# Kernel optimization log

Measured on AMD Instinct MI355X. Metric: run time of the kernel, lower is better.

## Reference

```python
import jax, jax.numpy as jnp
import numpy as np

N_OBJS = 100          # max detections / scatter buffer size
TOP_K = 100           # top_k_n peaks per channel
KP_THRES = 0.3        # score threshold before NMS
NMS_IOU = 0.5
RESIZE_H, RESIZE_W = 1536.0, 1536.0   # resize_shape (== heatmap HxW here)
H, W = 1536, 1536


def _peak_hms(hms):
    # 3x3 stride-1 SAME max pool; keep only local maxima (Base.apply_max_pool)
    hmax = jax.lax.reduce_window(hms, -jnp.inf, jax.lax.max, (1, 3, 3, 1), (1, 1, 1, 1), 'SAME')
    return jnp.where(hms == hmax, hms, 0.0)


def _top_k_loc(hms, k):
    # per-channel top-k peak coordinates -> [b, c, k, 2] (y, x) int32
    b, h, w, c = hms.shape
    flat = jnp.transpose(hms, (0, 3, 1, 2)).reshape(b, c, h * w)
    _, idx = jax.lax.top_k(flat, k)
    return jnp.stack([idx // w, idx % w], axis=-1).astype(jnp.int32)


def _iou_matrix(boxes):
    # boxes [N,4] = (y1,x1,y2,x2)
    y1, x1, y2, x2 = boxes[:, 0], boxes[:, 1], boxes[:, 2], boxes[:, 3]
    area = jnp.maximum(y2 - y1, 0.0) * jnp.maximum(x2 - x1, 0.0)
    iy1 = jnp.maximum(y1[:, None], y1[None, :]); ix1 = jnp.maximum(x1[:, None], x1[None, :])
    iy2 = jnp.minimum(y2[:, None], y2[None, :]); ix2 = jnp.minimum(x2[:, None], x2[None, :])
    inter = jnp.maximum(iy2 - iy1, 0.0) * jnp.maximum(ix2 - ix1, 0.0)
    union = area[:, None] + area[None, :] - inter
    return inter / jnp.maximum(union, 1e-8)


def _nms_single(boxes, scores):
    # greedy single-class NMS, fixed-size (combined_non_max_suppression equivalent,
    # clip_boxes=False, score_threshold=-inf); padded slots are zeros like TF.
    order = jnp.argsort(-scores)
    boxes, scores = boxes[order], scores[order]
    n = boxes.shape[0]
    iou = _iou_matrix(boxes)
    idxs = jnp.arange(n)

    def step(suppressed, inp):
        i, iou_row = inp
        keep_i = ~suppressed[i]
        return suppressed | (keep_i & (iou_row > NMS_IOU) & (idxs > i)), keep_i

    _, keep = jax.lax.scan(step, jnp.zeros(n, bool), (idxs, iou))
    perm = jnp.argsort(jnp.where(keep, 0, 1))  # stable: compact kept to front, score order preserved
    keep_s = keep[perm]
    out_boxes = jnp.where(keep_s[:, None], boxes[perm], 0.0)
    out_scores = jnp.where(keep_s, scores[perm], 0.0)
    return out_boxes, out_scores, jnp.zeros(n, jnp.float32)


def _forward(obj_heat_map, offset_map, size_maps, origin_shapes):
    resize_shape = jnp.array([RESIZE_H, RESIZE_W], jnp.float32)
    ratio = origin_shapes / resize_shape                      # [b,2]
    hms = _peak_hms(obj_heat_map)                             # [b,H,W,2]
    b = hms.shape[0]
    coors = _top_k_loc(hms, TOP_K)                            # [b,2,K,2]
    b_coors, b_lnmks = coors[:, :1], coors[:, 1:]             # obj / nose coords
    bidx = jnp.arange(b)[:, None, None]

    # nose landmark: scores at nose-channel peaks, masked mean of coords (int mean like TF)
    nose_scores = hms[bidx, b_lnmks[..., 0], b_lnmks[..., 1], 1]     # [b,1,K]
    nose_mask = nose_scores > 0.5
    cnt = jnp.maximum(jnp.sum(nose_mask), 1)
    lnmk_mean = jnp.sum(jnp.where(nose_mask[..., None], b_lnmks, 0), axis=(0, 1, 2)) // cnt
    b_lnmks_m = lnmk_mean.reshape(b, 1, 2)                    # requires b == 1 (as in original)
    b_nose_scores = jnp.where(nose_mask, nose_scores, -1.0).reshape(b, -1)

    # boxes from sizes at object peaks
    size_vals = size_maps[bidx, b_coors[..., 0], b_coors[..., 1]]    # [b,1,K,2]
    obj_scores = hms[bidx, b_coors[..., 0], b_coors[..., 1], 0]      # [b,1,K]
    centers = b_coors.astype(jnp.float32)
    tls = jnp.maximum(centers - size_vals / 2.0, 0.0)
    brs = jnp.minimum(centers + size_vals / 2.0, resize_shape - 1.0)
    bboxes = jnp.concatenate([tls, brs], axis=-1) * jnp.tile(ratio, (1, 2))[:, None, None, :]
    bboxes, scores = bboxes[:, 0], obj_scores[:, 0]           # [b,K,4], [b,K]

    # scatter masked candidates into -1-initialized buffer (tensor_scatter_nd_update equivalent)
    mask = scores > KP_THRES
    cand = jnp.where(mask[..., None], jnp.concatenate([bboxes, scores[..., None]], -1), -1.0)
    cand = jnp.pad(cand, ((0, 0), (0, N_OBJS - TOP_K), (0, 0)), constant_values=-1.0)  # [b,N_OBJS,5]

    nb, ns, nc = jax.vmap(_nms_single)(cand[..., :4], cand[..., 4])
    box_results = jnp.where(nb == -1.0, jnp.inf, nb)
    box_results = jnp.where(box_results == 0.0, jnp.inf, box_results)  # (x - 1 == -1)
    b_bboxes = jnp.concatenate([box_results, ns[..., None], nc[..., None]], axis=-1)  # [b,N_OBJS,6]

    # offset vectors at the mean nose landmark (gather 8ch -> [b,n,4,2])
    bidx2 = jnp.arange(b)[:, None]
    off = offset_map[bidx2, b_lnmks_m[..., 0], b_lnmks_m[..., 1]].reshape(b, 1, 4, 2)
    lf = b_lnmks_m.astype(jnp.float32)
    b_ENM = (lf[:, :, None, :] - off) * ratio[:, None, None, :]
    b_lnmks_out = lf * ratio[:, None, :]
    return b_bboxes, b_lnmks_out, b_ENM, b_nose_scores


def setup_inputs() -> dict:
    key = jax.random.key(0)
    k1, k2, k3 = jax.random.split(key, 3)
    obj_heat_map = jax.random.uniform(k1, (1, H, W, 2), jnp.float32)
    offset_map = jax.random.normal(k2, (1, H, W, 8), jnp.float32) * 8.0
    size_maps = jax.random.uniform(k3, (1, H, W, 2), jnp.float32) * 128.0
    origin_shapes = jnp.array([[1080.0, 1920.0]], jnp.float32)
    return {"obj_heat_map": obj_heat_map, "offset_map": offset_map,
            "size_maps": size_maps, "origin_shapes": origin_shapes}


def reference(obj_heat_map, offset_map, size_maps, origin_shapes):
    return _forward(obj_heat_map, offset_map, size_maps, origin_shapes)
```

## Files before the change

kernel.cpp:

```cpp
#include <hip/hip_runtime.h>
#include <cstdint>

#define IW 1536
#define IH 1536
#define TOPK 100
#define CAPP 327680
#define CAPB 128
#define CAPM 32768
#define BF_INF16 0x7F7Fu

typedef unsigned u32; typedef unsigned long long u64; typedef unsigned short u16;

#define OH1   0
#define OCNT  4096
#define OSEL  4100
#define OPK   4104
#define OPV   (OPK + 2*CAPP)
#define OMID  (OPV + CAPP)

__device__ __forceinline__ u32 enc16(u32 b){ b &= 0xFFFFu; return (b & 0x8000u) ? ((~b)&0xFFFFu) : (b|0x8000u); }
__device__ __forceinline__ u32 dec16(u32 e){ return (e & 0x8000u) ? (e^0x8000u) : ((~e)&0xFFFFu); }
__device__ __forceinline__ float up16(u32 b){ return __uint_as_float((b&0xFFFFu)<<16); }
__device__ __forceinline__ u16 f2bf(float f){ u32 u=__float_as_uint(f); return (u16)((u + 0x7FFFu + ((u>>16)&1u))>>16); }

__device__ __forceinline__ void wave_sel2048(const u32* bins, u32 need, int* Dout, u32* Aout){
  int lane = threadIdx.x & 63;
  u32 s = 0;
  #pragma unroll
  for(int k=0;k<32;++k) s += bins[lane*32+k];
  u32 c = s;
  #pragma unroll
  for(int off=1;off<64;off<<=1){
    u32 v = __shfl_down(c, off, 64);
    if(lane + off < 64) c += v;
  }
  u32 cnext = __shfl_down(c, 1, 64); if(lane==63) cnext = 0u;
  u64 m = __ballot(c >= need);
  if(m == 0ull){ if(lane==0){ *Dout = 0; *Aout = 0u; } return; }
  int L = 63 - __builtin_clzll((unsigned long long)m);
  if(lane == L){
    u32 above = cnext; int D = 32*L;
    for(int b=32*L+31; b>=32*L; --b){
      u32 h = bins[b];
      if(above + h >= need){ D = b; break; }
      above += h;
    }
    *Dout = D; *Aout = above;
  }
}

__global__ __launch_bounds__(1024) void scan_kernel(const u32* __restrict__ hm, u32* __restrict__ ws){
  __shared__ u32 lh[4096];
  __shared__ u32 lbuf[2][1600];
  __shared__ u16 vbuf[2][1600];
  __shared__ u32 lcnt[2], lbase[2];
  int tid = threadIdx.x, lane = tid & 63;
  for(int i=tid;i<4096;i+=1024) lh[i]=0u;
  if(tid<2) lcnt[tid]=0u;
  __syncthreads();

  int p = (blockIdx.x*1024 + tid)*4;
  int y = p / IW, x = p - y*IW;
  const u32* R1 = hm + y*IW;
  const u32* R0 = y ? R1 - IW : R1;
  const u32* R2 = (y < IH-1) ? R1 + IW : R1;
  uint4 c0 = *(const uint4*)(R0+x), c1 = *(const uint4*)(R1+x), c2 = *(const uint4*)(R2+x);
  int xl = x ? x-1 : 0, xr = (x+4 < IW) ? x+4 : IW-1;
  u32 a0[6] = {R0[xl], c0.x, c0.y, c0.z, c0.w, R0[xr]};
  u32 a1[6] = {R1[xl], c1.x, c1.y, c1.z, c1.w, R1[xr]};
  u32 a2[6] = {R2[xl], c2.x, c2.y, c2.z, c2.w, R2[xr]};

  #pragma unroll
  for(int j=0;j<4;++j){
    u32 cc = a1[j+1];
    u32 cl = cc & 0xFFFFu, chv = cc >> 16;
    u32 m0=0u, m1=0u;
    #pragma unroll
    for(int d=0;d<3;++d){
      u32 n0=a0[j+d], n2=a2[j+d]; u32 t;
      t=n0&0xFFFFu; m0=t>m0?t:m0;  t=n0>>16; m1=t>m1?t:m1;
      t=n2&0xFFFFu; m0=t>m0?t:m0;  t=n2>>16; m1=t>m1?t:m1;
    }
    { u32 n=a1[j];   u32 t=n&0xFFFFu; m0=t>m0?t:m0; t=n>>16; m1=t>m1?t:m1; }
    { u32 n=a1[j+2]; u32 t=n&0xFFFFu; m0=t>m0?t:m0; t=n>>16; m1=t>m1?t:m1; }
    bool pk0 = (cl >= m0), pk1 = (chv >= m1);
    u32 idx = (u32)(p + j);

    u64 mk0 = __ballot(pk0);
    if(mk0){
      u32 cw = __popcll(mk0), b;
      if(lane==0) b = atomicAdd(&lcnt[0], cw);
      b = __shfl(b, 0);
      if(pk0){
        u32 pos = b + __popcll(mk0 & ((1ull<<lane)-1ull));
        if(pos < 1600){ lbuf[0][pos] = idx; vbuf[0][pos] = (u16)cl; }
      }
    }
    u64 mk1 = __ballot(pk1);
    if(mk1){
      u32 cw = __popcll(mk1), b;
      if(lane==0) b = atomicAdd(&lcnt[1], cw);
      b = __shfl(b, 0);
      if(pk1){
        u32 pos = b + __popcll(mk1 & ((1ull<<lane)-1ull));
        if(pos < 1600){ lbuf[1][pos] = idx; vbuf[1][pos] = (u16)chv; }
      }
    }
    if(pk0) atomicAdd(&lh[enc16(cl)>>5], 1u);
    if(pk1) atomicAdd(&lh[2048 + (enc16(chv)>>5)], 1u);
  }
  __syncthreads();
  if(tid < 2){
    u32 n = lcnt[tid]; if(n > 1600) n = 1600;
    lcnt[tid] = n;
    lbase[tid] = atomicAdd(&ws[OCNT+tid], n);
  }
  __syncthreads();
  u16* pv = (u16*)(ws + OPV);
  for(int ch=0;ch<2;++ch){
    u32 n = lcnt[ch], base = lbase[ch];
    for(u32 i=tid;i<n;i+=1024){
      u32 g = base + i;
      if(g < CAPP){ ws[OPK + ch*CAPP + g] = lbuf[ch][i]; pv[ch*CAPP + g] = vbuf[ch][i]; }
    }
  }
  for(int i=tid;i<4096;i+=1024) if(lh[i]) atomicAdd(&ws[OH1+i], lh[i]);
}

#define GRID2 128
__global__ __launch_bounds__(1024) void mid_kernel(u32* __restrict__ ws){
  __shared__ u32 lhh[4096];
  __shared__ u64 mbuf[2][2048];
  __shared__ u32 mcnt[2], mbase[2];
  __shared__ int Dsh[2]; __shared__ u32 Ash[2];
  int tid = threadIdx.x, lane = tid & 63;
  for(int i=tid;i<4096;i+=1024) lhh[i] = ws[OH1+i];
  if(tid < 2) mcnt[tid] = 0u;
  __syncthreads();
  if(tid < 64)                wave_sel2048(lhh,        (u32)TOPK, &Dsh[0], &Ash[0]);
  else if(tid < 128)          wave_sel2048(lhh + 2048, (u32)TOPK, &Dsh[1], &Ash[1]);
  __syncthreads();
  if(blockIdx.x == 0 && tid < 2){ ws[OSEL+tid] = (u32)Dsh[tid]; ws[OSEL+2+tid] = Ash[tid]; }

  const u16* pv = (const u16*)(ws + OPV);
  for(int ch=0;ch<2;++ch){
    u32 n = ws[OCNT+ch]; if(n > CAPP) n = CAPP;
    int D = Dsh[ch];
    for(u32 base = blockIdx.x*1024; base < n; base += GRID2*1024){
      u32 i = base + tid;
      bool act = (i < n);
      u32 e = 0, idx = 0;
      if(act){ e = enc16(pv[ch*CAPP + i]); idx = ws[OPK + ch*CAPP + i]; }
      bool hit = act && ((int)(e>>5) >= D);
      u64 mk = __ballot(hit);
      if(mk){
        u32 cw = __popcll(mk), b;
        if(lane==0) b = atomicAdd(&mcnt[ch], cw);
        b = __shfl(b, 0);
        if(hit){
          u32 pos = b + __popcll(mk & ((1ull<<lane)-1ull));
          if(pos < 2048) mbuf[ch][pos] = ((u64)e<<32) | (u32)(~idx);
        }
      }
    }
  }
  __syncthreads();
  if(tid < 2){
    u32 c = mcnt[tid]; if(c > 2048) c = 2048;
    mcnt[tid] = c;
    mbase[tid] = atomicAdd(&ws[OCNT+2+tid], c);
  }
  __syncthreads();
  u64* mid = (u64*)(ws + OMID);
  for(int ch=0;ch<2;++ch)
    for(u32 i=tid;i<mcnt[ch];i+=1024){
      u32 g = mbase[ch] + i;
      if(g < CAPM) mid[ch*CAPM + g] = mbuf[ch][i];
    }
}

__global__ __launch_bounds__(1024) void finalize_kernel(
    u32* __restrict__ ws, const u32* __restrict__ szm, const u16* __restrict__ offm,
    const u16* __restrict__ orig, u16* __restrict__ out){
  __shared__ u64 keys[CAPB];
  __shared__ u32 lsdw[16][32];
  __shared__ u32 lsd[32];
  __shared__ u32 h2[2048];
  __shared__ u32 wbits[64];
  __shared__ u32 sel[CAPB];
  __shared__ int Bv, selc, selc2, Lsh;
  __shared__ float oval[TOPK]; __shared__ int oidx[TOPK];
  __shared__ float nval[TOPK]; __shared__ int nidx[TOPK];
  __shared__ float cbox[TOPK][4]; __shared__ float cscore[TOPK]; __shared__ float area[TOPK];
  __shared__ int sup[TOPK]; __shared__ int slotv[TOPK];
  __shared__ u64 nbits[2*TOPK];
  __shared__ u64 suppS[2];
  __shared__ int cS, srS, scS, meanr, meanc;
  int tid = threadIdx.x, lane = tid & 63, wid = tid >> 6;

  if(tid < TOPK){ oval[tid]=0.0f; oidx[tid]=0; nval[tid]=0.0f; nidx[tid]=0; }
  __syncthreads();

  for(int ch=0; ch<2; ++ch){
    int nM = (int)ws[OCNT+2+ch]; if(nM > CAPM) nM = CAPM;
    int D = (int)ws[OSEL+ch];
    u32 above = ws[OSEL+2+ch];
    const u64* mid = ((const u64*)(ws + OMID)) + ch*CAPM;
    float* dval = ch ? nval : oval;
    int*   didx = ch ? nidx : oidx;

    for(int i=tid;i<2048;i+=1024) h2[i]=0u;
    if(tid < 512) ((u32*)lsdw)[tid] = 0u;
    if(tid < 64) wbits[tid]=0u;
    if(tid == 0){ selc = 0; selc2 = 0; Bv = 0; Lsh = 0; }
    __syncthreads();

    for(int i=tid;i<nM;i+=1024){
      u64 k = mid[i]; u32 e = (u32)(k>>32);
      if((int)(e>>5) > D){
        int pos = atomicAdd(&selc, 1); if(pos < CAPB) keys[pos] = k;
      } else {
        atomicAdd(&lsdw[wid][e & 31u], 1u);
      }
    }
    __syncthreads();
    if(tid < 32){
      u32 s = 0;
      #pragma unroll
      for(int w=0;w<16;++w) s += lsdw[w][tid];
      lsd[tid] = s;
    }
    __syncthreads();
    if(tid == 0){
      u32 need2 = (u32)TOPK - above;
      u32 a2 = 0; int L = 0;
      for(int b=31;b>=1;--b){
        u32 h = lsd[b];
        if(a2 + h >= need2){ L = b; break; }
        a2 += h;
      }
      Lsh = L;
    }
    __syncthreads();
    u32 thr = ((u32)D<<5) | (u32)Lsh;
    float tval = up16(dec16(thr));

    for(int i=tid;i<nM;i+=1024){
      u64 k = mid[i]; u32 e = (u32)(k>>32);
      if(e > thr && (e>>5) == (u32)D){
        int pos = atomicAdd(&selc, 1); if(pos < CAPB) keys[pos] = k;
      } else if(e == thr){
        u32 idx = ~(u32)(k & 0xFFFFFFFFu);
        atomicAdd(&h2[idx>>11], 1u);
      }
    }
    __syncthreads();
    int nA = selc; if(nA > CAPB) nA = CAPB; if(nA > TOPK) nA = TOPK;
    if(tid < nA){
      u64 kreg = keys[tid];
      int r = 0;
      for(int j=0;j<nA;++j) r += (keys[j] > kreg);
      if(r < TOPK){
        dval[r] = up16(dec16((u32)(kreg>>32)));
        didx[r] = (int)(~(u32)(kreg & 0xFFFFFFFFu));
      }
    }
    int need = TOPK - nA;

    if(need > 0){
      if(tid < 64){
        int base = tid*32;
        u32 s = 0;
        #pragma unroll
        for(int k2=0;k2<32;++k2) s += h2[base+k2];
        u32 c = s;
        #pragma unroll
        for(int off=1;off<64;off<<=1){
          u32 v = __shfl_up(c, off, 64);
          if(lane >= off) c += v;
        }
        u64 m = __ballot(c >= (u32)need);
        int L = (int)(__ffsll((unsigned long long)m) - 1);
        if(tid == L){
          u32 cum2 = c - s;
          int B = base;
          for(int k2=0;k2<32;++k2){
            u32 hb = h2[base+k2];
            if(cum2 + hb >= (u32)need){ B = base+k2; break; }
            cum2 += hb;
          }
          Bv = B;
        }
      }
      __syncthreads();
      int B = Bv;
      for(int i=tid;i<nM;i+=1024){
        u64 k = mid[i]; u32 e = (u32)(k>>32);
        if(e == thr){
          u32 idx = ~(u32)(k & 0xFFFFFFFFu);
          int b = (int)(idx>>11);
          if(b < B){
            int pos = atomicAdd(&selc2, 1);
            if(pos < CAPB) sel[pos] = idx;
          } else if(b == B){
            atomicOr(&wbits[(idx&2047)>>5], 1u<<(idx&31));
          }
        }
      }
      __syncthreads();
      int sc = selc2; if(sc > CAPB) sc = CAPB;
      if(tid < sc){
        u32 v = sel[tid];
        int r = 0;
        for(int j=0;j<sc;++j) r += (sel[j] < v);
        if(nA + r < TOPK){ dval[nA+r] = tval; didx[nA+r] = (int)v; }
      }
      if(tid == 0){
        int rem = need - sc;
        int pos = nA + sc;
        for(int wi=0; wi<64 && rem>0; ++wi){
          u32 bits = wbits[wi];
          while(bits && rem>0){
            int l = __ffs(bits) - 1;
            bits &= bits - 1;
            if(pos < TOPK){ dval[pos] = tval; didx[pos] = (int)(((u32)Bv<<11) | ((u32)wi<<5) | (u32)l); }
            ++pos; --rem;
          }
        }
      }
    }
    __syncthreads();
  }

  float ry = up16(orig[0]) / 1536.0f;
  float rx = up16(orig[1]) / 1536.0f;

  if(tid == 0){ cS = 0; srS = 0; scS = 0; }
  __syncthreads();
  if(tid < TOPK && nval[tid] > 0.5f){
    atomicAdd(&cS, 1);
    atomicAdd(&srS, nidx[tid] / IW);
    atomicAdd(&scS, nidx[tid] % IW);
  }
  if(tid < TOPK) out[610 + tid] = f2bf(nval[tid] > 0.5f ? nval[tid] : -1.0f);
  __syncthreads();
  if(tid == 0){
    int c = cS < 1 ? 1 : cS;
    meanr = srS / c; meanc = scS / c;
  }

  if(tid < TOPK){
    int idx = oidx[tid];
    int r = idx / IW, c = idx - r*IW;
    float score = oval[tid];
    u32 sz = szm[idx];
    float sy = up16(sz), sx = up16(sz>>16);
    float cy = (float)r, cx = (float)c;
    float tly = fmaxf(cy - sy*0.5f, 0.0f);
    float tlx = fmaxf(cx - sx*0.5f, 0.0f);
    float bry = fminf(cy + sy*0.5f, 1535.0f);
    float brx = fminf(cx + sx*0.5f, 1535.0f);
    bool mk = score > 0.3f;
    float b0 = mk ? tly*ry : -1.0f;
    float b1 = mk ? tlx*rx : -1.0f;
    float b2 = mk ? bry*ry : -1.0f;
    float b3 = mk ? brx*rx : -1.0f;
    cbox[tid][0]=b0; cbox[tid][1]=b1; cbox[tid][2]=b2; cbox[tid][3]=b3;
    cscore[tid] = mk ? score : -1.0f;
    area[tid] = fmaxf(b2-b0,0.0f) * fmaxf(b3-b1,0.0f);
  }
  if(tid < 2*TOPK) nbits[tid] = 0ull;
  __syncthreads();

  for(int t=tid; t<TOPK*TOPK; t+=1024){
    int i = t / TOPK, j = t - i*TOPK;
    if(j > i){
      float iy1 = fmaxf(cbox[i][0], cbox[j][0]);
      float ix1 = fmaxf(cbox[i][1], cbox[j][1]);
      float iy2 = fminf(cbox[i][2], cbox[j][2]);
      float ix2 = fminf(cbox[i][3], cbox[j][3]);
      float inter = fmaxf(iy2-iy1,0.0f) * fmaxf(ix2-ix1,0.0f);
      float uni = (area[i] + area[j]) - inter;
      if(inter / fmaxf(uni, 1e-8f) > 0.5f)
        atomicOr(&nbits[i*2 + (j>>6)], 1ull << (j&63));
    }
  }
  __syncthreads();
  if(tid == 0){
    u64 s0 = 0ull, s1 = 0ull;
    for(int i=0;i<TOPK;++i){
      bool su = (i<64) ? ((s0>>i)&1ull) : ((s1>>(i-64))&1ull);
      if(!su){ s0 |= nbits[i*2]; s1 |= nbits[i*2+1]; }
    }
    suppS[0] = s0; suppS[1] = s1;
  }
  __syncthreads();
  if(tid < TOPK) sup[tid] = (int)((suppS[tid>>6] >> (tid&63)) & 1ull);
  __syncthreads();

  if(tid < TOPK){
    int kbefore = 0, sbefore = 0, ktot = 0;
    for(int j=0;j<TOPK;++j){
      int sj = sup[j];
      ktot += (1 - sj);
      if(j < tid){ kbefore += (1 - sj); sbefore += sj; }
    }
    int slot = sup[tid] ? (ktot + sbefore) : kbefore;
    slotv[slot] = tid;
  }
  __syncthreads();

  if(tid < TOPK){
    int s = slotv[tid];
    bool ks = !sup[s];
    u16 row[6];
    if(ks){
      for(int d=0;d<4;++d){
        float v = cbox[s][d];
        row[d] = (v == -1.0f || v == 0.0f) ? (u16)BF_INF16 : f2bf(v);
      }
      row[4] = f2bf(cscore[s]);
    } else {
      for(int d=0;d<4;++d) row[d] = (u16)BF_INF16;
      row[4] = 0;
    }
    row[5] = 0;
    for(int d=0;d<6;++d) out[tid*6 + d] = row[d];
  }

  if(tid == 0){
    float lfy = (float)meanr, lfx = (float)meanc;
    out[600] = f2bf(lfy * ry);
    out[601] = f2bf(lfx * rx);
    const u16* op = offm + ((size_t)meanr*IW + meanc)*8;
    for(int p=0;p<4;++p){
      out[602 + p*2 + 0] = f2bf((lfy - up16(op[p*2+0])) * ry);
      out[602 + p*2 + 1] = f2bf((lfx - up16(op[p*2+1])) * rx);
    }
  }
}

extern "C" void kernel_launch(void* const* d_in, const int* in_sizes, int n_in,
                              void* d_out, int out_size, void* d_ws, size_t ws_size,
                              hipStream_t stream) {
  const u32* heat = (const u32*)d_in[0];
  const u16* offm = (const u16*)d_in[1];
  const u32* szm  = (const u32*)d_in[2];
  const u16* orig = (const u16*)d_in[3];
  u16* out = (u16*)d_out;
  u32* ws = (u32*)d_ws;

  hipMemsetAsync(ws, 0, 4104*sizeof(u32), stream);
  scan_kernel<<<576, 1024, 0, stream>>>(heat, ws);
  mid_kernel<<<GRID2, 1024, 0, stream>>>(ws);
  finalize_kernel<<<1, 1024, 0, stream>>>(ws, szm, offm, orig, out);
}
```

Before: 200.3 us.

## Split mid candidates into above-digit list and tie list with global low-digit histogram

After: 199.3 us. No clear change (-0.5%).

```diff
diff --git a/kernel.cpp b/kernel.cpp
--- a/kernel.cpp
+++ b/kernel.cpp
@@ -6,17 +6,20 @@
 #define TOPK 100
 #define CAPP 327680
 #define CAPB 128
-#define CAPM 32768
+#define CAPT 8192
 #define BF_INF16 0x7F7Fu
 
 typedef unsigned u32; typedef unsigned long long u64; typedef unsigned short u16;
 
 #define OH1   0
 #define OCNT  4096
-#define OSEL  4100
-#define OPK   4104
+#define OSEL  4102
+#define OLSD  4106
+#define OZEND 4172
+#define OPK   4172
 #define OPV   (OPK + 2*CAPP)
-#define OMID  (OPV + CAPP)
+#define OLB   (OPV + CAPP)
+#define OLT   (OLB + 4*CAPB)
 
 __device__ __forceinline__ u32 enc16(u32 b){ b &= 0xFFFFu; return (b & 0x8000u) ? ((~b)&0xFFFFu) : (b|0x8000u); }
 __device__ __forceinline__ u32 dec16(u32 e){ return (e & 0x8000u) ? (e^0x8000u) : ((~e)&0xFFFFu); }
@@ -130,19 +133,22 @@
 #define GRID2 128
 __global__ __launch_bounds__(1024) void mid_kernel(u32* __restrict__ ws){
   __shared__ u32 lhh[4096];
-  __shared__ u64 mbuf[2][2048];
-  __shared__ u32 mcnt[2], mbase[2];
+  __shared__ u64 tbuf[2][2048];
+  __shared__ u32 tcnt[2], tbase[2];
+  __shared__ u32 lsdl[64];
   __shared__ int Dsh[2]; __shared__ u32 Ash[2];
   int tid = threadIdx.x, lane = tid & 63;
   for(int i=tid;i<4096;i+=1024) lhh[i] = ws[OH1+i];
-  if(tid < 2) mcnt[tid] = 0u;
-  __syncthreads();
-  if(tid < 64)                wave_sel2048(lhh,        (u32)TOPK, &Dsh[0], &Ash[0]);
-  else if(tid < 128)          wave_sel2048(lhh + 2048, (u32)TOPK, &Dsh[1], &Ash[1]);
+  if(tid < 2) tcnt[tid] = 0u;
+  if(tid < 64) lsdl[tid] = 0u;
+  __syncthreads();
+  if(tid < 64)       wave_sel2048(lhh,        (u32)TOPK, &Dsh[0], &Ash[0]);
+  else if(tid < 128) wave_sel2048(lhh + 2048, (u32)TOPK, &Dsh[1], &Ash[1]);
   __syncthreads();
   if(blockIdx.x == 0 && tid < 2){ ws[OSEL+tid] = (u32)Dsh[tid]; ws[OSEL+2+tid] = Ash[tid]; }
 
   const u16* pv = (const u16*)(ws + OPV);
+  u64* listB = (u64*)(ws + OLB);
   for(int ch=0;ch<2;++ch){
     u32 n = ws[OCNT+ch]; if(n > CAPP) n = CAPP;
     int D = Dsh[ch];
@@ -151,40 +157,45 @@
       bool act = (i < n);
       u32 e = 0, idx = 0;
       if(act){ e = enc16(pv[ch*CAPP + i]); idx = ws[OPK + ch*CAPP + i]; }
-      bool hit = act && ((int)(e>>5) >= D);
-      u64 mk = __ballot(hit);
+      if(act && (int)(e>>5) > D){
+        u32 pos = atomicAdd(&ws[OCNT+2+ch], 1u);
+        if(pos < CAPB) listB[ch*CAPB + pos] = ((u64)e<<32) | (u32)(~idx);
+      }
+      bool isT = act && ((int)(e>>5) == D);
+      if(isT) atomicAdd(&lsdl[ch*32 + (e & 31u)], 1u);
+      u64 mk = __ballot(isT);
       if(mk){
         u32 cw = __popcll(mk), b;
-        if(lane==0) b = atomicAdd(&mcnt[ch], cw);
+        if(lane==0) b = atomicAdd(&tcnt[ch], cw);
         b = __shfl(b, 0);
-        if(hit){
+        if(isT){
           u32 pos = b + __popcll(mk & ((1ull<<lane)-1ull));
-          if(pos < 2048) mbuf[ch][pos] = ((u64)e<<32) | (u32)(~idx);
+          if(pos < 2048) tbuf[ch][pos] = ((u64)e<<32) | (u32)(~idx);
         }
       }
     }
   }
   __syncthreads();
   if(tid < 2){
-    u32 c = mcnt[tid]; if(c > 2048) c = 2048;
-    mcnt[tid] = c;
-    mbase[tid] = atomicAdd(&ws[OCNT+2+tid], c);
-  }
-  __syncthreads();
-  u64* mid = (u64*)(ws + OMID);
+    u32 c = tcnt[tid]; if(c > 2048) c = 2048;
+    tcnt[tid] = c;
+    tbase[tid] = atomicAdd(&ws[OCNT+4+tid], c);
+  }
+  __syncthreads();
+  u64* tie = (u64*)(ws + OLT);
   for(int ch=0;ch<2;++ch)
-    for(u32 i=tid;i<mcnt[ch];i+=1024){
-      u32 g = mbase[ch] + i;
-      if(g < CAPM) mid[ch*CAPM + g] = mbuf[ch][i];
-    }
+    for(u32 i=tid;i<tcnt[ch];i+=1024){
+      u32 g = tbase[ch] + i;
+      if(g < CAPT) tie[ch*CAPT + g] = tbuf[ch][i];
+    }
+  if(tid < 64 && lsdl[tid]) atomicAdd(&ws[OLSD + tid], lsdl[tid]);
 }
 
-__global__ __launch_bounds__(1024) void finalize_kernel(
+__global__ __launch_bounds__(256) void finalize_kernel(
     u32* __restrict__ ws, const u32* __restrict__ szm, const u16* __restrict__ offm,
     const u16* __restrict__ orig, u16* __restrict__ out){
+  __shared__ u64 tl[CAPT];
   __shared__ u64 keys[CAPB];
-  __shared__ u32 lsdw[16][32];
-  __shared__ u32 lsd[32];
   __shared__ u32 h2[2048];
   __shared__ u32 wbits[64];
   __shared__ u32 sel[CAPB];
@@ -196,46 +207,30 @@
   __shared__ u64 nbits[2*TOPK];
   __shared__ u64 suppS[2];
   __shared__ int cS, srS, scS, meanr, meanc;
-  int tid = threadIdx.x, lane = tid & 63, wid = tid >> 6;
+  int tid = threadIdx.x, lane = tid & 63;
 
   if(tid < TOPK){ oval[tid]=0.0f; oidx[tid]=0; nval[tid]=0.0f; nidx[tid]=0; }
   __syncthreads();
 
   for(int ch=0; ch<2; ++ch){
-    int nM = (int)ws[OCNT+2+ch]; if(nM > CAPM) nM = CAPM;
-    int D = (int)ws[OSEL+ch];
+    int nB = (int)ws[OCNT+2+ch]; if(nB > CAPB) nB = CAPB;
+    int nT = (int)ws[OCNT+4+ch]; if(nT > CAPT) nT = CAPT;
+    int D  = (int)ws[OSEL+ch];
     u32 above = ws[OSEL+2+ch];
-    const u64* mid = ((const u64*)(ws + OMID)) + ch*CAPM;
+    const u64* listB = ((const u64*)(ws + OLB)) + ch*CAPB;
+    const u64* tie   = ((const u64*)(ws + OLT)) + ch*CAPT;
     float* dval = ch ? nval : oval;
     int*   didx = ch ? nidx : oidx;
 
-    for(int i=tid;i<2048;i+=1024) h2[i]=0u;
-    if(tid < 512) ((u32*)lsdw)[tid] = 0u;
+    for(int i=tid;i<nT;i+=256) tl[i] = tie[i];
+    for(int i=tid;i<2048;i+=256) h2[i]=0u;
     if(tid < 64) wbits[tid]=0u;
-    if(tid == 0){ selc = 0; selc2 = 0; Bv = 0; Lsh = 0; }
-    __syncthreads();
-
-    for(int i=tid;i<nM;i+=1024){
-      u64 k = mid[i]; u32 e = (u32)(k>>32);
-      if((int)(e>>5) > D){
-        int pos = atomicAdd(&selc, 1); if(pos < CAPB) keys[pos] = k;
-      } else {
-        atomicAdd(&lsdw[wid][e & 31u], 1u);
-      }
-    }
-    __syncthreads();
-    if(tid < 32){
-      u32 s = 0;
-      #pragma unroll
-      for(int w=0;w<16;++w) s += lsdw[w][tid];
-      lsd[tid] = s;
-    }
-    __syncthreads();
     if(tid == 0){
+      selc = 0; selc2 = 0; Bv = 0;
       u32 need2 = (u32)TOPK - above;
       u32 a2 = 0; int L = 0;
       for(int b=31;b>=1;--b){
-        u32 h = lsd[b];
+        u32 h = ws[OLSD + ch*32 + b];
         if(a2 + h >= need2){ L = b; break; }
         a2 += h;
       }
@@ -245,9 +240,12 @@
     u32 thr = ((u32)D<<5) | (u32)Lsh;
     float tval = up16(dec16(thr));
 
-    for(int i=tid;i<nM;i+=1024){
-      u64 k = mid[i]; u32 e = (u32)(k>>32);
-      if(e > thr && (e>>5) == (u32)D){
+    for(int i=tid;i<nB;i+=256){
+      int pos = atomicAdd(&selc, 1); if(pos < CAPB) keys[pos] = listB[i];
+    }
+    for(int i=tid;i<nT;i+=256){
+      u64 k = tl[i]; u32 e = (u32)(k>>32);
+      if(e > thr){
         int pos = atomicAdd(&selc, 1); if(pos < CAPB) keys[pos] = k;
       } else if(e == thr){
         u32 idx = ~(u32)(k & 0xFFFFFFFFu);
@@ -294,8 +292,8 @@
       }
       __syncthreads();
       int B = Bv;
-      for(int i=tid;i<nM;i+=1024){
-        u64 k = mid[i]; u32 e = (u32)(k>>32);
+      for(int i=tid;i<nT;i+=256){
+        u64 k = tl[i]; u32 e = (u32)(k>>32);
         if(e == thr){
           u32 idx = ~(u32)(k & 0xFFFFFFFFu);
           int b = (int)(idx>>11);
@@ -372,7 +370,7 @@
   if(tid < 2*TOPK) nbits[tid] = 0ull;
   __syncthreads();
 
-  for(int t=tid; t<TOPK*TOPK; t+=1024){
+  for(int t=tid; t<TOPK*TOPK; t+=256){
     int i = t / TOPK, j = t - i*TOPK;
     if(j > i){
       float iy1 = fmaxf(cbox[i][0], cbox[j][0]);
@@ -450,8 +448,8 @@
   u16* out = (u16*)d_out;
   u32* ws = (u32*)d_ws;
 
-  hipMemsetAsync(ws, 0, 4104*sizeof(u32), stream);
+  hipMemsetAsync(ws, 0, OZEND*sizeof(u32), stream);
   scan_kernel<<<576, 1024, 0, stream>>>(heat, ws);
   mid_kernel<<<GRID2, 1024, 0, stream>>>(ws);
-  finalize_kernel<<<1, 1024, 0, stream>>>(ws, szm, offm, orig, out);
+  finalize_kernel<<<1, 256, 0, stream>>>(ws, szm, offm, orig, out);
 }
```
